# Optimization experiments

Hardware: AMD Instinct MI355X
Metric: run time of the kernel (lower is better)

Reference implementation:

```python
import jax, jax.numpy as jnp
import numpy as np

IN_F = 4096
OUT_F = 4096
B, S = 4, 2048
BITS = 4
N_LEVELS = 1 << BITS  # 16


def setup_inputs() -> dict:
    key = jax.random.key(0)
    kx, kr, ks, kb = jax.random.split(key, 4)
    x = jax.random.normal(kx, (B, S, IN_F), dtype=jnp.float32)
    # random orthogonal rotation (TurboQuantMSE rotation matrix, seeded)
    g = jax.random.normal(kr, (IN_F, IN_F), dtype=jnp.float32)
    rotation, _ = jnp.linalg.qr(g)
    # 4-bit scalar codebook: Lloyd-Max-style Gaussian levels, scaled for
    # unit-norm rows whose rotated entries ~ N(0, 1/in_features)
    p = (jnp.arange(N_LEVELS, dtype=jnp.float32) + 0.5) / N_LEVELS
    levels = jnp.sqrt(2.0) * jax.scipy.special.erfinv(2.0 * p - 1.0)
    codebook = (levels / jnp.sqrt(jnp.float32(IN_F))).astype(jnp.float32)
    weight_indices = jax.random.randint(jax.random.fold_in(key, 1), (OUT_F, IN_F), 0, N_LEVELS, dtype=jnp.int32)
    weight_scale = jax.random.uniform(ks, (OUT_F,), dtype=jnp.float32, minval=0.5, maxval=2.0)
    bias = jax.random.normal(kb, (OUT_F,), dtype=jnp.float32)
    return {"x": x, "weight_indices": weight_indices, "weight_scale": weight_scale,
            "bias": bias, "rotation": rotation, "codebook": codebook}


def reference(x, weight_indices, weight_scale, bias, rotation, codebook):
    # dequantize: codebook lookup -> inverse rotation -> per-row rescale
    w_rot = codebook[weight_indices]                      # (out, in)
    w_hat = jnp.einsum('oi,ji->oj', w_rot, rotation)      # apply R^T: (out, in)
    w = w_hat * weight_scale[:, None]                     # (out, in)
    # F.linear: x @ W^T + b
    return jnp.einsum('bsi,oi->bso', x, w) + bias
```

## Files before the change

kernel.cpp:

```cpp
#include <hip/hip_runtime.h>

typedef short short8 __attribute__((ext_vector_type(8)));
typedef float f32x4 __attribute__((ext_vector_type(4)));

#define GLOBAL_AS __attribute__((address_space(1)))
#define LDS_AS    __attribute__((address_space(3)))

__device__ __forceinline__ unsigned short f2bf(float f) {
    unsigned u = __builtin_bit_cast(unsigned, f);
    u += 0x7fffu + ((u >> 16) & 1u);
    return (unsigned short)(u >> 16);
}

__global__ __launch_bounds__(256) void k_idx2bf(const int* __restrict__ idx,
                                                const float* __restrict__ cb,
                                                ushort* __restrict__ out, int n4) {
    int i = blockIdx.x * 256 + threadIdx.x;
    if (i >= n4) return;
    int4 v = reinterpret_cast<const int4*>(idx)[i];
    ushort4 o;
    o.x = f2bf(cb[v.x]); o.y = f2bf(cb[v.y]);
    o.z = f2bf(cb[v.z]); o.w = f2bf(cb[v.w]);
    reinterpret_cast<ushort4*>(out)[i] = o;
}

__global__ __launch_bounds__(256) void k_f2bf(const float* __restrict__ in,
                                              ushort* __restrict__ out, int n4) {
    int i = blockIdx.x * 256 + threadIdx.x;
    if (i >= n4) return;
    float4 v = reinterpret_cast<const float4*>(in)[i];
    ushort4 o;
    o.x = f2bf(v.x); o.y = f2bf(v.y); o.z = f2bf(v.z); o.w = f2bf(v.w);
    reinterpret_cast<ushort4*>(out)[i] = o;
}

template <int EPI>
__global__ __launch_bounds__(256, 2) void gemm_bt(const ushort* __restrict__ A,
                                                  const ushort* __restrict__ B,
                                                  void* __restrict__ C,
                                                  const float* __restrict__ extra) {
    constexpr int BM = 128, BN = 128, BK = 64;
    constexpr int K = 4096, N = 4096;

    __shared__ ushort sA[BM * BK];
    __shared__ ushort sB[BN * BK];

    const int tid  = threadIdx.x;
    const int w    = tid >> 6;
    const int lane = tid & 63;
    const int m0 = blockIdx.y * BM;
    const int n0 = blockIdx.x * BN;

    const int srow = lane >> 3;
    const int scol = (lane & 7) * 8;
    const ushort* gA = A + (size_t)(m0 + srow) * K + scol;
    const ushort* gB = B + (size_t)(n0 + srow) * K + scol;

    const int fr = lane & 15;
    const int fk = (lane >> 4) * 8;
    const int wr = (w >> 1) * 64;
    const int wc = (w & 1) * 64;

    f32x4 zero = {0.f, 0.f, 0.f, 0.f};
    f32x4 acc[4][4];
#pragma unroll
    for (int i = 0; i < 4; ++i)
#pragma unroll
        for (int j = 0; j < 4; ++j) acc[i][j] = zero;

    for (int kt = 0; kt < K / BK; ++kt) {
        const int kb = kt * BK;
#pragma unroll
        for (int i = 0; i < 4; ++i) {
            const int row0 = i * 32 + w * 8;
            __builtin_amdgcn_global_load_lds(
                (const GLOBAL_AS void*)(gA + (size_t)row0 * K + kb),
                (LDS_AS void*)(sA + row0 * BK), 16, 0, 0);
            __builtin_amdgcn_global_load_lds(
                (const GLOBAL_AS void*)(gB + (size_t)row0 * K + kb),
                (LDS_AS void*)(sB + row0 * BK), 16, 0, 0);
        }
        __syncthreads();

#pragma unroll
        for (int kk = 0; kk < BK; kk += 32) {
            short8 af[4], bfr[4];
#pragma unroll
            for (int mi = 0; mi < 4; ++mi)
                af[mi] = *reinterpret_cast<const short8*>(sA + (wr + mi * 16 + fr) * BK + kk + fk);
#pragma unroll
            for (int ni = 0; ni < 4; ++ni)
                bfr[ni] = *reinterpret_cast<const short8*>(sB + (wc + ni * 16 + fr) * BK + kk + fk);
#pragma unroll
            for (int mi = 0; mi < 4; ++mi)
#pragma unroll
                for (int ni = 0; ni < 4; ++ni)
                    acc[mi][ni] = __builtin_amdgcn_mfma_f32_16x16x32_bf16(
                        af[mi], bfr[ni], acc[mi][ni], 0, 0, 0);
        }
        __syncthreads();
    }

    const int rbase = m0 + wr + ((lane >> 4) * 4);
    const int cbase = n0 + wc + (lane & 15);
    if (EPI == 0) {
        ushort* Cw = (ushort*)C;
#pragma unroll
        for (int mi = 0; mi < 4; ++mi) {
#pragma unroll
            for (int r = 0; r < 4; ++r) {
                const int row = rbase + mi * 16 + r;
                const float s = extra[row];
#pragma unroll
                for (int ni = 0; ni < 4; ++ni) {
                    const int col = cbase + ni * 16;
                    Cw[(size_t)row * N + col] = f2bf(acc[mi][ni][r] * s);
                }
            }
        }
    } else {
        float* Cf = (float*)C;
#pragma unroll
        for (int ni = 0; ni < 4; ++ni) {
            const int col = cbase + ni * 16;
            const float b = extra[col];
#pragma unroll
            for (int mi = 0; mi < 4; ++mi) {
#pragma unroll
                for (int r = 0; r < 4; ++r) {
                    const int row = rbase + mi * 16 + r;
                    Cf[(size_t)row * N + col] = acc[mi][ni][r] + b;
                }
            }
        }
    }
}

extern "C" void kernel_launch(void* const* d_in, const int* in_sizes, int n_in,
                              void* d_out, int out_size, void* d_ws, size_t ws_size,
                              hipStream_t stream) {
    const float* x     = (const float*)d_in[0];
    const int*   widx  = (const int*)  d_in[1];
    const float* wscal = (const float*)d_in[2];
    const float* bias  = (const float*)d_in[3];
    const float* rot   = (const float*)d_in[4];
    const float* cb    = (const float*)d_in[5];
    float* out = (float*)d_out;

    constexpr size_t IN_F = 4096, OUT_F = 4096, MTOK = 8192;
    char* ws = (char*)d_ws;
    ushort* wq = (ushort*)(ws);
    ushort* rb = (ushort*)(ws + 33554432);
    ushort* xb = (ushort*)(ws + 67108864);
    ushort* wb = (ushort*)(ws + 134217728);
    (void)ws_size; (void)in_sizes; (void)n_in; (void)out_size;

    {
        int n4 = (int)(OUT_F * IN_F / 4);
        k_idx2bf<<<n4 / 256, 256, 0, stream>>>(widx, cb, wq, n4);
        k_f2bf<<<n4 / 256, 256, 0, stream>>>(rot, rb, n4);
        int n4x = (int)(MTOK * IN_F / 4);
        k_f2bf<<<n4x / 256, 256, 0, stream>>>(x, xb, n4x);
    }

    gemm_bt<0><<<dim3(4096 / 128, 4096 / 128), 256, 0, stream>>>(wq, rb, (void*)wb, wscal);

    gemm_bt<1><<<dim3(4096 / 128, 8192 / 128), 256, 0, stream>>>(xb, wb, (void*)out, bias);
}
```

Measured before the change: 525.3 us.

## Rewrite GEMM as 256x256 tile, 8-wave double-buffered pipelined kernel

Replaces the 128x128 single-buffered GEMM with a 256x256 tile, 512-thread kernel. It double-buffers LDS and splits each K step into four compute phases, issuing global-to-LDS loads for the next tiles between them with explicit barriers, setprio and waitcnt control. It also adds an XOR swizzle on LDS addresses to avoid bank conflicts and remaps blocks for L2 locality. The aim is to overlap memory traffic with MFMA work and raise arithmetic intensity, at the cost of more registers and 128KB LDS per block, which limits occupancy.

```diff
diff --git a/kernel.cpp b/kernel.cpp
--- a/kernel.cpp
+++ b/kernel.cpp
@@ -34,102 +34,150 @@
     reinterpret_cast<ushort4*>(out)[i] = o;
 }
 
+
+#define CH_AE(j) ((((j) & 8) << 1) | ((j) & 7))
+#define CH_AL(j) (CH_AE(j) + 8)
+#define CH_BE(j) ((((j) & 12) << 1) | ((j) & 3))
+#define CH_BL(j) (CH_BE(j) + 4)
+
+#define STAGE2(G, LDSBASE, KB, CF) do {                                         \
+    const int c0_ = CF(2 * w), c1_ = CF(2 * w + 1);                             \
+    __builtin_amdgcn_global_load_lds(                                           \
+        (const GLOBAL_AS void*)((G) + (size_t)(c0_ * 8 + srow8) * 4096 + (KB) + scol), \
+        (LDS_AS void*)((LDSBASE) + c0_ * 512), 16, 0, 0);                       \
+    __builtin_amdgcn_global_load_lds(                                           \
+        (const GLOBAL_AS void*)((G) + (size_t)(c1_ * 8 + srow8) * 4096 + (KB) + scol), \
+        (LDS_AS void*)((LDSBASE) + c1_ * 512), 16, 0, 0);                       \
+} while (0)
+
+#define PHASE(MH, NH, ...) do {                                                 \
+    short8 af_[2][4], bf_[2][2];                                                \
+    _Pragma("unroll")                                                           \
+    for (int k2 = 0; k2 < 2; ++k2) {                                            \
+        _Pragma("unroll")                                                       \
+        for (int mi = 0; mi < 4; ++mi) {                                        \
+            const int lb = (arow + (MH) * 64 + mi * 16) * 128 + k2 * 64 + fkb;  \
+            af_[k2][mi] = *reinterpret_cast<const short8*>((const char*)At + (lb ^ swb)); \
+        }                                                                       \
+        _Pragma("unroll")                                                       \
+        for (int ni = 0; ni < 2; ++ni) {                                        \
+            const int lb = (brow + (NH) * 32 + ni * 16) * 128 + k2 * 64 + fkb;  \
+            bf_[k2][ni] = *reinterpret_cast<const short8*>((const char*)Bt + (lb ^ swb)); \
+        }                                                                       \
+    }                                                                           \
+    __VA_ARGS__;                                                                \
+    asm volatile("" ::: "memory");                                              \
+    __builtin_amdgcn_s_barrier();                                               \
+    __builtin_amdgcn_s_setprio(1);                                              \
+    __builtin_amdgcn_sched_barrier(0);                                          \
+    _Pragma("unroll")                                                           \
+    for (int k2 = 0; k2 < 2; ++k2)                                              \
+        _Pragma("unroll")                                                       \
+        for (int mi = 0; mi < 4; ++mi)                                          \
+            _Pragma("unroll")                                                   \
+            for (int ni = 0; ni < 2; ++ni)                                      \
+                acc[(MH) * 4 + mi][(NH) * 2 + ni] =                             \
+                    __builtin_amdgcn_mfma_f32_16x16x32_bf16(                    \
+                        af_[k2][mi], bf_[k2][ni], acc[(MH) * 4 + mi][(NH) * 2 + ni], 0, 0, 0); \
+    __builtin_amdgcn_sched_barrier(0);                                          \
+    __builtin_amdgcn_s_setprio(0);                                              \
+    asm volatile("" ::: "memory");                                              \
+    __builtin_amdgcn_s_barrier();                                               \
+    asm volatile("" ::: "memory");                                              \
+} while (0)
+
 template <int EPI>
-__global__ __launch_bounds__(256, 2) void gemm_bt(const ushort* __restrict__ A,
+__global__ __launch_bounds__(512, 2) void gemm256(const ushort* __restrict__ A,
                                                   const ushort* __restrict__ B,
                                                   void* __restrict__ C,
                                                   const float* __restrict__ extra) {
-    constexpr int BM = 128, BN = 128, BK = 64;
-    constexpr int K = 4096, N = 4096;
-
-    __shared__ ushort sA[BM * BK];
-    __shared__ ushort sB[BN * BK];
+    constexpr int K = 4096, N = 4096, NT = K / 64;
+    __shared__ ushort sA[2][256 * 64];
+    __shared__ ushort sB[2][256 * 64];
 
     const int tid  = threadIdx.x;
     const int w    = tid >> 6;
     const int lane = tid & 63;
-    const int m0 = blockIdx.y * BM;
-    const int n0 = blockIdx.x * BN;
-
-    const int srow = lane >> 3;
-    const int scol = (lane & 7) * 8;
-    const ushort* gA = A + (size_t)(m0 + srow) * K + scol;
-    const ushort* gB = B + (size_t)(n0 + srow) * K + scol;
-
-    const int fr = lane & 15;
-    const int fk = (lane >> 4) * 8;
-    const int wr = (w >> 1) * 64;
-    const int wc = (w & 1) * 64;
-
-    f32x4 zero = {0.f, 0.f, 0.f, 0.f};
-    f32x4 acc[4][4];
-#pragma unroll
-    for (int i = 0; i < 4; ++i)
-#pragma unroll
-        for (int j = 0; j < 4; ++j) acc[i][j] = zero;
-
-    for (int kt = 0; kt < K / BK; ++kt) {
-        const int kb = kt * BK;
-#pragma unroll
-        for (int i = 0; i < 4; ++i) {
-            const int row0 = i * 32 + w * 8;
-            __builtin_amdgcn_global_load_lds(
-                (const GLOBAL_AS void*)(gA + (size_t)row0 * K + kb),
-                (LDS_AS void*)(sA + row0 * BK), 16, 0, 0);
-            __builtin_amdgcn_global_load_lds(
-                (const GLOBAL_AS void*)(gB + (size_t)row0 * K + kb),
-                (LDS_AS void*)(sB + row0 * BK), 16, 0, 0);
-        }
-        __syncthreads();
-
-#pragma unroll
-        for (int kk = 0; kk < BK; kk += 32) {
-            short8 af[4], bfr[4];
-#pragma unroll
-            for (int mi = 0; mi < 4; ++mi)
-                af[mi] = *reinterpret_cast<const short8*>(sA + (wr + mi * 16 + fr) * BK + kk + fk);
-#pragma unroll
-            for (int ni = 0; ni < 4; ++ni)
-                bfr[ni] = *reinterpret_cast<const short8*>(sB + (wc + ni * 16 + fr) * BK + kk + fk);
-#pragma unroll
-            for (int mi = 0; mi < 4; ++mi)
-#pragma unroll
-                for (int ni = 0; ni < 4; ++ni)
-                    acc[mi][ni] = __builtin_amdgcn_mfma_f32_16x16x32_bf16(
-                        af[mi], bfr[ni], acc[mi][ni], 0, 0, 0);
-        }
-        __syncthreads();
+    const int wm = w >> 2, wn = w & 3;
+
+    const int nwg = gridDim.x;
+    const int sw  = ((int)blockIdx.x & 7) * (nwg >> 3) + ((int)blockIdx.x >> 3);
+    const int m0 = (sw >> 4) * 256;
+    const int n0 = (sw & 15) * 256;
+
+    const ushort* gA = A + (size_t)m0 * K;
+    const ushort* gB = B + (size_t)n0 * K;
+
+    const int srow8 = lane >> 3;
+    const int scol  = ((lane & 7) * 8) ^ (((lane >> 5) & 1) << 4);
+
+    const int fr   = lane & 15;
+    const int fkb  = ((lane >> 4) & 3) * 16;
+    const int swb  = ((fr >> 2) & 1) << 5;
+    const int arow = wm * 128 + fr;
+    const int brow = wn * 64 + fr;
+
+    f32x4 acc[8][4];
+#pragma unroll
+    for (int i = 0; i < 8; ++i)
+#pragma unroll
+        for (int j = 0; j < 4; ++j) acc[i][j] = (f32x4){0.f, 0.f, 0.f, 0.f};
+
+    STAGE2(gA, sA[0], 0, CH_AE);  STAGE2(gB, sB[0], 0, CH_BE);
+    STAGE2(gA, sA[0], 0, CH_AL);  STAGE2(gB, sB[0], 0, CH_BL);
+    STAGE2(gA, sA[1], 64, CH_AE); STAGE2(gB, sB[1], 64, CH_BE);
+    asm volatile("s_waitcnt vmcnt(4)" ::: "memory");
+    __builtin_amdgcn_s_barrier();
+    asm volatile("" ::: "memory");
+
+    for (int t = 0; t < NT; ++t) {
+        const int cur = t & 1;
+        const ushort* At = sA[cur];
+        const ushort* Bt = sB[cur];
+        ushort* nxA = sA[cur ^ 1];
+        ushort* nxB = sB[cur ^ 1];
+        ushort* ccA = sA[cur];
+        ushort* ccB = sB[cur];
+        const int kb1 = (t + 1) * 64, kb2 = (t + 2) * 64;
+        const bool st1 = (t + 1) < NT, st2 = (t + 2) < NT;
+
+        PHASE(0, 0, if (st1) STAGE2(gA, nxA, kb1, CH_AL));
+        PHASE(0, 1, if (st1) STAGE2(gB, nxB, kb1, CH_BL));
+        PHASE(1, 0, if (st2) STAGE2(gA, ccA, kb2, CH_AE));
+        PHASE(1, 1, if (st2) STAGE2(gB, ccB, kb2, CH_BE));
+
+        if (st2) asm volatile("s_waitcnt vmcnt(4)" ::: "memory");
+        else     asm volatile("s_waitcnt vmcnt(0)" ::: "memory");
+        __builtin_amdgcn_s_barrier();
+        asm volatile("" ::: "memory");
     }
 
-    const int rbase = m0 + wr + ((lane >> 4) * 4);
-    const int cbase = n0 + wc + (lane & 15);
+    const int rb = m0 + wm * 128 + ((lane >> 4) * 4);
+    const int cb = n0 + wn * 64 + (lane & 15);
     if (EPI == 0) {
         ushort* Cw = (ushort*)C;
 #pragma unroll
-        for (int mi = 0; mi < 4; ++mi) {
+        for (int mi = 0; mi < 8; ++mi) {
 #pragma unroll
             for (int r = 0; r < 4; ++r) {
-                const int row = rbase + mi * 16 + r;
+                const int row = rb + mi * 16 + r;
                 const float s = extra[row];
 #pragma unroll
-                for (int ni = 0; ni < 4; ++ni) {
-                    const int col = cbase + ni * 16;
-                    Cw[(size_t)row * N + col] = f2bf(acc[mi][ni][r] * s);
-                }
+                for (int ni = 0; ni < 4; ++ni)
+                    Cw[(size_t)row * N + cb + ni * 16] = f2bf(acc[mi][ni][r] * s);
             }
         }
     } else {
         float* Cf = (float*)C;
 #pragma unroll
         for (int ni = 0; ni < 4; ++ni) {
-            const int col = cbase + ni * 16;
-            const float b = extra[col];
-#pragma unroll
-            for (int mi = 0; mi < 4; ++mi) {
+            const float b = extra[cb + ni * 16];
+#pragma unroll
+            for (int mi = 0; mi < 8; ++mi) {
 #pragma unroll
                 for (int r = 0; r < 4; ++r) {
-                    const int row = rbase + mi * 16 + r;
-                    Cf[(size_t)row * N + col] = acc[mi][ni][r] + b;
+                    const int row = rb + mi * 16 + r;
+                    Cf[(size_t)row * N + cb + ni * 16] = acc[mi][ni][r] + b;
                 }
             }
         }
@@ -149,21 +197,21 @@
 
     constexpr size_t IN_F = 4096, OUT_F = 4096, MTOK = 8192;
     char* ws = (char*)d_ws;
-    ushort* wq = (ushort*)(ws);
-    ushort* rb = (ushort*)(ws + 33554432);
-    ushort* xb = (ushort*)(ws + 67108864);
-    ushort* wb = (ushort*)(ws + 134217728);
+    ushort* wq   = (ushort*)(ws);
+    ushort* rbuf = (ushort*)(ws + 33554432);
+    ushort* xb   = (ushort*)(ws + 67108864);
+    ushort* wb   = (ushort*)(ws + 134217728);
     (void)ws_size; (void)in_sizes; (void)n_in; (void)out_size;
 
     {
         int n4 = (int)(OUT_F * IN_F / 4);
         k_idx2bf<<<n4 / 256, 256, 0, stream>>>(widx, cb, wq, n4);
-        k_f2bf<<<n4 / 256, 256, 0, stream>>>(rot, rb, n4);
+        k_f2bf<<<n4 / 256, 256, 0, stream>>>(rot, rbuf, n4);
         int n4x = (int)(MTOK * IN_F / 4);
         k_f2bf<<<n4x / 256, 256, 0, stream>>>(x, xb, n4x);
     }
 
-    gemm_bt<0><<<dim3(4096 / 128, 4096 / 128), 256, 0, stream>>>(wq, rb, (void*)wb, wscal);
-
-    gemm_bt<1><<<dim3(4096 / 128, 8192 / 128), 256, 0, stream>>>(xb, wb, (void*)out, bias);
-}
+    gemm256<0><<<dim3(256), 512, 0, stream>>>(wq, rbuf, (void*)wb, wscal);
+
+    gemm256<1><<<dim3(512), 512, 0, stream>>>(xb, wb, (void*)out, bias);
+}
```

New measurement: 660.6 us. 25.7% more time.
